# Optimization experiments

Measured on AMD Instinct MI355X. Metric: run time of the kernel, lower is better.

## Reference

```python
import jax, jax.numpy as jnp
import numpy as np

B, S, D = 4, 2048, 1024


def setup_inputs() -> dict:
    key = jax.random.key(0)
    ks = jax.random.split(key, 7)
    s = 1.0 / np.sqrt(D)
    return {
        "x": jax.random.normal(ks[0], (B, S, D), dtype=jnp.float32),
        "Wq": jax.random.normal(ks[1], (D, D), dtype=jnp.float32) * s,
        "bq": jax.random.normal(ks[2], (D,), dtype=jnp.float32) * s,
        "Wk": jax.random.normal(ks[3], (D, D), dtype=jnp.float32) * s,
        "bk": jax.random.normal(ks[4], (D,), dtype=jnp.float32) * s,
        "Wv": jax.random.normal(ks[5], (D, D), dtype=jnp.float32) * s,
        "bv": jax.random.normal(ks[6], (D,), dtype=jnp.float32) * s,
    }


def reference(x, Wq, bq, Wk, bk, Wv, bv):
    # Linear layers: y = x @ W^T + b (torch nn.Linear convention)
    Q = jnp.einsum("bsd,ed->bse", x, Wq) + bq  # [B,S,D]
    K = jnp.einsum("bsd,ed->bse", x, Wk) + bk
    V = jnp.einsum("bsd,ed->bse", x, Wv) + bv
    d = x.shape[-1]
    scores = jnp.einsum("bqd,bkd->bqk", Q, K) / jnp.sqrt(jnp.float32(d))  # [B,S,S]
    weights = jax.nn.softmax(scores, axis=-1)
    O = jnp.einsum("bqk,bkd->bqd", weights, V)  # [B,S,D]
    return O
```

## Files before the change

### kernel.cpp

```cpp
#include <hip/hip_runtime.h>

typedef __bf16 bf16x8 __attribute__((ext_vector_type(8)));
typedef __bf16 bf16x4 __attribute__((ext_vector_type(4)));
typedef float  f32x4  __attribute__((ext_vector_type(4)));

#define BM 128
#define BN 128
#define BK 32

__device__ __forceinline__ void gload_lds16(const __bf16* g, __bf16* l) {
  __builtin_amdgcn_global_load_lds(
      (const __attribute__((address_space(1))) void*)g,
      (__attribute__((address_space(3))) void*)l,
      16, 0, 0);
}

__global__ void cvt_f32_bf16(const float* __restrict__ s, __bf16* __restrict__ d, int n4) {
  int i = blockIdx.x * 256 + threadIdx.x;
  if (i < n4) {
    float4 v = ((const float4*)s)[i];
    bf16x4 o;
    o[0] = (__bf16)v.x; o[1] = (__bf16)v.y; o[2] = (__bf16)v.z; o[3] = (__bf16)v.w;
    ((bf16x4*)d)[i] = o;
  }
}

__global__ void cvt_weights(const float* __restrict__ Wq, const float* __restrict__ Wk,
                            const float* __restrict__ Wv,
                            __bf16* __restrict__ Wqk, __bf16* __restrict__ Wvb) {
  const int mat = blockIdx.x >> 10;
  const int i = (blockIdx.x & 1023) * 256 + threadIdx.x;
  const float* src = (mat == 0) ? Wq : (mat == 1) ? Wk : Wv;
  __bf16* dst = (mat == 0) ? Wqk : (mat == 1) ? (Wqk + 1048576) : Wvb;
  float4 v = ((const float4*)src)[i];
  bf16x4 o;
  o[0] = (__bf16)v.x; o[1] = (__bf16)v.y; o[2] = (__bf16)v.z; o[3] = (__bf16)v.w;
  ((bf16x4*)dst)[i] = o;
}

template<int MODE>
__global__ __launch_bounds__(256, 2)
void gemm_bt(const __bf16* __restrict__ A, const __bf16* __restrict__ B,
             float* __restrict__ C,
             int lda, int ldb, int ldc, int K,
             long sA, long sB, long sC,
             const float* __restrict__ bias0, const float* __restrict__ bias1,
             __bf16* __restrict__ out0, __bf16* __restrict__ out1)
{
  A += (long)blockIdx.z * sA;
  B += (long)blockIdx.z * sB;

  const int tid  = threadIdx.x;
  const int wave = tid >> 6;
  const int lane = tid & 63;
  const int quad = lane >> 4;
  const int l15  = lane & 15;
  const int bm0  = blockIdx.x * BM;
  const int bn0  = blockIdx.y * BN;
  const int wm   = (wave >> 1) * 64;
  const int wn   = (wave & 1) * 64;

  __shared__ __align__(16) __bf16 As[BM * BK];
  __shared__ __align__(16) __bf16 Bs[BN * BK];

  f32x4 acc[4][4];
#pragma unroll
  for (int i = 0; i < 4; ++i)
#pragma unroll
    for (int j = 0; j < 4; ++j)
      acc[i][j] = (f32x4){0.f, 0.f, 0.f, 0.f};

  const int l0 = tid * 8;
  const int l1 = (256 + tid) * 8;
  const int r0 = l0 >> 5, c0 = l0 & 31;
  const int r1 = l1 >> 5, c1 = l1 & 31;
  const __bf16* Ag0 = A + (size_t)(bm0 + r0) * lda + c0;
  const __bf16* Ag1 = A + (size_t)(bm0 + r1) * lda + c1;
  const __bf16* Bg0 = B + (size_t)(bn0 + r0) * ldb + c0;
  const __bf16* Bg1 = B + (size_t)(bn0 + r1) * ldb + c1;

  for (int k0 = 0; k0 < K; k0 += BK) {
    gload_lds16(Ag0 + k0, &As[l0]);
    gload_lds16(Ag1 + k0, &As[l1]);
    gload_lds16(Bg0 + k0, &Bs[l0]);
    gload_lds16(Bg1 + k0, &Bs[l1]);
    __syncthreads();

    bf16x8 af[4], bfv[4];
#pragma unroll
    for (int i = 0; i < 4; ++i)
      af[i] = *(const bf16x8*)&As[(wm + i * 16 + l15) * BK + quad * 8];
#pragma unroll
    for (int i = 0; i < 4; ++i)
      bfv[i] = *(const bf16x8*)&Bs[(wn + i * 16 + l15) * BK + quad * 8];

#pragma unroll
    for (int mi = 0; mi < 4; ++mi)
#pragma unroll
      for (int ni = 0; ni < 4; ++ni)
        acc[mi][ni] = __builtin_amdgcn_mfma_f32_16x16x32_bf16(
            af[mi], bfv[ni], acc[mi][ni], 0, 0, 0);
    __syncthreads();
  }

#pragma unroll
  for (int mi = 0; mi < 4; ++mi) {
#pragma unroll
    for (int ni = 0; ni < 4; ++ni) {
      const int gn = bn0 + wn + ni * 16 + l15;
#pragma unroll
      for (int r = 0; r < 4; ++r) {
        const int gm = bm0 + wm + mi * 16 + quad * 4 + r;
        float v = acc[mi][ni][r];
        if (MODE == 0) {
          const int mat = gn >> 10;
          const int d   = gn & 1023;
          const float* bias = (mat == 0) ? bias0 : bias1;
          __bf16* dst = (mat == 0) ? out0 : out1;
          dst[(size_t)gm * 1024 + d] = (__bf16)(v + bias[d]);
        } else if (MODE == 1) {
          const int b = gn >> 11, s = gn & 2047;
          out0[(size_t)b * (1024 * 2048) + (size_t)gm * 2048 + s] =
              (__bf16)(v + bias0[gm]);
        } else {
          C[(long)blockIdx.z * sC + (size_t)gm * ldc + gn] = v;
        }
      }
    }
  }
}

__global__ __launch_bounds__(256)
void softmax_rows(float* __restrict__ S) {
  float* row = S + (size_t)blockIdx.x * 2048;
  __bf16* wrow = (__bf16*)row;
  const int t = threadIdx.x;
  const int wave = t >> 6;
  const int lane = t & 63;
  __shared__ float redm[4];
  __shared__ float reds[4];

  float4 a = ((const float4*)row)[t];
  float4 b = ((const float4*)row)[t + 256];
  const float sc = 0.03125f;
  float x0 = a.x * sc, x1 = a.y * sc, x2 = a.z * sc, x3 = a.w * sc;
  float x4 = b.x * sc, x5 = b.y * sc, x6 = b.z * sc, x7 = b.w * sc;

  float mx = fmaxf(fmaxf(fmaxf(x0, x1), fmaxf(x2, x3)),
                   fmaxf(fmaxf(x4, x5), fmaxf(x6, x7)));
#pragma unroll
  for (int off = 32; off > 0; off >>= 1)
    mx = fmaxf(mx, __shfl_down(mx, off));
  if (lane == 0) redm[wave] = mx;
  __syncthreads();
  mx = fmaxf(fmaxf(redm[0], redm[1]), fmaxf(redm[2], redm[3]));

  float e0 = __expf(x0 - mx), e1 = __expf(x1 - mx);
  float e2 = __expf(x2 - mx), e3 = __expf(x3 - mx);
  float e4 = __expf(x4 - mx), e5 = __expf(x5 - mx);
  float e6 = __expf(x6 - mx), e7 = __expf(x7 - mx);
  float s = ((e0 + e1) + (e2 + e3)) + ((e4 + e5) + (e6 + e7));
#pragma unroll
  for (int off = 32; off > 0; off >>= 1)
    s += __shfl_down(s, off);
  if (lane == 0) reds[wave] = s;
  __syncthreads();
  const float rinv = 1.0f / (((reds[0] + reds[1]) + (reds[2] + reds[3])));

  bf16x4 w0, w1;
  w0[0] = (__bf16)(e0 * rinv); w0[1] = (__bf16)(e1 * rinv);
  w0[2] = (__bf16)(e2 * rinv); w0[3] = (__bf16)(e3 * rinv);
  w1[0] = (__bf16)(e4 * rinv); w1[1] = (__bf16)(e5 * rinv);
  w1[2] = (__bf16)(e6 * rinv); w1[3] = (__bf16)(e7 * rinv);
  ((bf16x4*)wrow)[t] = w0;
  ((bf16x4*)wrow)[t + 256] = w1;
}

extern "C" void kernel_launch(void* const* d_in, const int* in_sizes, int n_in,
                              void* d_out, int out_size, void* d_ws, size_t ws_size,
                              hipStream_t stream) {
  const float* x  = (const float*)d_in[0];
  const float* Wq = (const float*)d_in[1];
  const float* bq = (const float*)d_in[2];
  const float* Wk = (const float*)d_in[3];
  const float* bk = (const float*)d_in[4];
  const float* Wv = (const float*)d_in[5];
  const float* bv = (const float*)d_in[6];
  float* out = (float*)d_out;

  char* ws = (char*)d_ws;
  __bf16* Q    = (__bf16*)(ws);
  __bf16* Kb   = (__bf16*)(ws + (16ull << 20));
  __bf16* Vt   = (__bf16*)(ws + (32ull << 20));
  __bf16* xb   = (__bf16*)(ws + (48ull << 20));
  __bf16* Wqk  = (__bf16*)(ws + (64ull << 20));
  __bf16* Wvb  = (__bf16*)(ws + (68ull << 20));
  float*  Sc   = (float*)(ws + (48ull << 20));

  cvt_f32_bf16<<<8192, 256, 0, stream>>>(x, xb, 8388608 / 4);
  cvt_weights<<<3072, 256, 0, stream>>>(Wq, Wk, Wv, Wqk, Wvb);

  dim3 blk(256);
  gemm_bt<0><<<dim3(64, 16, 1), blk, 0, stream>>>(
      xb, Wqk, nullptr, 1024, 1024, 0, 1024,
      0L, 0L, 0L, bq, bk, Q, Kb);

  gemm_bt<1><<<dim3(8, 64, 1), blk, 0, stream>>>(
      Wvb, xb, nullptr, 1024, 1024, 0, 1024,
      0L, 0L, 0L, bv, nullptr, Vt, nullptr);

  gemm_bt<2><<<dim3(16, 16, 4), blk, 0, stream>>>(
      Q, Kb, Sc, 1024, 1024, 2048, 1024,
      2048L * 1024, 2048L * 1024, 2048L * 2048,
      nullptr, nullptr, nullptr, nullptr);

  softmax_rows<<<8192, 256, 0, stream>>>(Sc);

  gemm_bt<2><<<dim3(16, 8, 4), blk, 0, stream>>>(
      (const __bf16*)Sc, Vt, out, 4096, 2048, 1024, 2048,
      2048L * 4096, 1024L * 2048, 2048L * 1024,
      nullptr, nullptr, nullptr, nullptr);
}
```

Before: 283.0 us.

## Merge conversion and QKV projection launches, use narrower tiles for PV GEMM

```diff
diff --git a/kernel.cpp b/kernel.cpp
--- a/kernel.cpp
+++ b/kernel.cpp
@@ -15,23 +15,23 @@
       16, 0, 0);
 }
 
-__global__ void cvt_f32_bf16(const float* __restrict__ s, __bf16* __restrict__ d, int n4) {
-  int i = blockIdx.x * 256 + threadIdx.x;
-  if (i < n4) {
-    float4 v = ((const float4*)s)[i];
-    bf16x4 o;
-    o[0] = (__bf16)v.x; o[1] = (__bf16)v.y; o[2] = (__bf16)v.z; o[3] = (__bf16)v.w;
-    ((bf16x4*)d)[i] = o;
-  }
-}
-
-__global__ void cvt_weights(const float* __restrict__ Wq, const float* __restrict__ Wk,
-                            const float* __restrict__ Wv,
-                            __bf16* __restrict__ Wqk, __bf16* __restrict__ Wvb) {
-  const int mat = blockIdx.x >> 10;
-  const int i = (blockIdx.x & 1023) * 256 + threadIdx.x;
-  const float* src = (mat == 0) ? Wq : (mat == 1) ? Wk : Wv;
-  __bf16* dst = (mat == 0) ? Wqk : (mat == 1) ? (Wqk + 1048576) : Wvb;
+__global__ void cvt_all(const float* __restrict__ x, const float* __restrict__ Wq,
+                        const float* __restrict__ Wk, const float* __restrict__ Wv,
+                        __bf16* __restrict__ xb, __bf16* __restrict__ Wqk,
+                        __bf16* __restrict__ Wvb) {
+  int b = blockIdx.x;
+  const float* src;
+  __bf16* dst;
+  int i;
+  if (b < 8192) {
+    src = x; dst = xb; i = b * 256 + threadIdx.x;
+  } else {
+    b -= 8192;
+    const int mat = b >> 10;
+    i = (b & 1023) * 256 + threadIdx.x;
+    src = (mat == 0) ? Wq : (mat == 1) ? Wk : Wv;
+    dst = (mat == 0) ? Wqk : (mat == 1) ? (Wqk + 1048576) : Wvb;
+  }
   float4 v = ((const float4*)src)[i];
   bf16x4 o;
   o[0] = (__bf16)v.x; o[1] = (__bf16)v.y; o[2] = (__bf16)v.z; o[3] = (__bf16)v.w;
@@ -45,18 +45,30 @@
              int lda, int ldb, int ldc, int K,
              long sA, long sB, long sC,
              const float* __restrict__ bias0, const float* __restrict__ bias1,
-             __bf16* __restrict__ out0, __bf16* __restrict__ out1)
+             const float* __restrict__ bias2, const __bf16* __restrict__ Wvb,
+             __bf16* __restrict__ out0, __bf16* __restrict__ out1,
+             __bf16* __restrict__ out2)
 {
-  A += (long)blockIdx.z * sA;
-  B += (long)blockIdx.z * sB;
+  const __bf16* Ap = A + (long)blockIdx.z * sA;
+  const __bf16* Bp = B + (long)blockIdx.z * sB;
+
+  int bx, by;
+  if (MODE == 3) {
+    const int gid = blockIdx.x;
+    if (gid < 1024) { bx = gid & 63; by = gid >> 6; }
+    else { const int g = gid - 1024; bx = g & 7; by = g >> 3;
+           Ap = Wvb; Bp = A; }
+  } else {
+    bx = blockIdx.x; by = blockIdx.y;
+  }
 
   const int tid  = threadIdx.x;
   const int wave = tid >> 6;
   const int lane = tid & 63;
   const int quad = lane >> 4;
   const int l15  = lane & 15;
-  const int bm0  = blockIdx.x * BM;
-  const int bn0  = blockIdx.y * BN;
+  const int bm0  = bx * BM;
+  const int bn0  = by * BN;
   const int wm   = (wave >> 1) * 64;
   const int wn   = (wave & 1) * 64;
 
@@ -68,6 +80,96 @@
   for (int i = 0; i < 4; ++i)
 #pragma unroll
     for (int j = 0; j < 4; ++j)
+      acc[i][j] = (f32x4){0.f, 0.f, 0.f, 0.f};
+
+  const int l0 = tid * 8;
+  const int l1 = (256 + tid) * 8;
+  const int r0 = l0 >> 5, c0 = l0 & 31;
+  const int r1 = l1 >> 5, c1 = l1 & 31;
+  const __bf16* Ag0 = Ap + (size_t)(bm0 + r0) * lda + c0;
+  const __bf16* Ag1 = Ap + (size_t)(bm0 + r1) * lda + c1;
+  const __bf16* Bg0 = Bp + (size_t)(bn0 + r0) * ldb + c0;
+  const __bf16* Bg1 = Bp + (size_t)(bn0 + r1) * ldb + c1;
+
+  for (int k0 = 0; k0 < K; k0 += BK) {
+    gload_lds16(Ag0 + k0, &As[l0]);
+    gload_lds16(Ag1 + k0, &As[l1]);
+    gload_lds16(Bg0 + k0, &Bs[l0]);
+    gload_lds16(Bg1 + k0, &Bs[l1]);
+    __syncthreads();
+
+    bf16x8 af[4], bfv[4];
+#pragma unroll
+    for (int i = 0; i < 4; ++i)
+      af[i] = *(const bf16x8*)&As[(wm + i * 16 + l15) * BK + quad * 8];
+#pragma unroll
+    for (int i = 0; i < 4; ++i)
+      bfv[i] = *(const bf16x8*)&Bs[(wn + i * 16 + l15) * BK + quad * 8];
+
+#pragma unroll
+    for (int mi = 0; mi < 4; ++mi)
+#pragma unroll
+      for (int ni = 0; ni < 4; ++ni)
+        acc[mi][ni] = __builtin_amdgcn_mfma_f32_16x16x32_bf16(
+            af[mi], bfv[ni], acc[mi][ni], 0, 0, 0);
+    __syncthreads();
+  }
+
+#pragma unroll
+  for (int mi = 0; mi < 4; ++mi) {
+#pragma unroll
+    for (int ni = 0; ni < 4; ++ni) {
+      const int gn = bn0 + wn + ni * 16 + l15;
+#pragma unroll
+      for (int r = 0; r < 4; ++r) {
+        const int gm = bm0 + wm + mi * 16 + quad * 4 + r;
+        float v = acc[mi][ni][r];
+        if (MODE == 3) {
+          if (blockIdx.x < 1024) {
+            const int mat = gn >> 10;
+            const int d   = gn & 1023;
+            const float* bias = (mat == 0) ? bias0 : bias1;
+            __bf16* dst = (mat == 0) ? out0 : out1;
+            dst[(size_t)gm * 1024 + d] = (__bf16)(v + bias[d]);
+          } else {
+            const int b = gn >> 11, s = gn & 2047;
+            out2[(size_t)b * (1024 * 2048) + (size_t)gm * 2048 + s] =
+                (__bf16)(v + bias2[gm]);
+          }
+        } else {
+          C[(long)blockIdx.z * sC + (size_t)gm * ldc + gn] = v;
+        }
+      }
+    }
+  }
+}
+
+__global__ __launch_bounds__(256, 4)
+void gemm_pv(const __bf16* __restrict__ A, const __bf16* __restrict__ B,
+             float* __restrict__ C,
+             int lda, int ldb, int ldc, int K, long sA, long sB, long sC)
+{
+  A += (long)blockIdx.z * sA;
+  B += (long)blockIdx.z * sB;
+
+  const int tid  = threadIdx.x;
+  const int wave = tid >> 6;
+  const int lane = tid & 63;
+  const int quad = lane >> 4;
+  const int l15  = lane & 15;
+  const int bm0  = blockIdx.x * 128;
+  const int bn0  = blockIdx.y * 64;
+  const int wm   = (wave >> 1) * 64;
+  const int wn   = (wave & 1) * 32;
+
+  __shared__ __align__(16) __bf16 As[128 * BK];
+  __shared__ __align__(16) __bf16 Bs[64 * BK];
+
+  f32x4 acc[4][2];
+#pragma unroll
+  for (int i = 0; i < 4; ++i)
+#pragma unroll
+    for (int j = 0; j < 2; ++j)
       acc[i][j] = (f32x4){0.f, 0.f, 0.f, 0.f};
 
   const int l0 = tid * 8;
@@ -77,27 +179,25 @@
   const __bf16* Ag0 = A + (size_t)(bm0 + r0) * lda + c0;
   const __bf16* Ag1 = A + (size_t)(bm0 + r1) * lda + c1;
   const __bf16* Bg0 = B + (size_t)(bn0 + r0) * ldb + c0;
-  const __bf16* Bg1 = B + (size_t)(bn0 + r1) * ldb + c1;
 
   for (int k0 = 0; k0 < K; k0 += BK) {
     gload_lds16(Ag0 + k0, &As[l0]);
     gload_lds16(Ag1 + k0, &As[l1]);
     gload_lds16(Bg0 + k0, &Bs[l0]);
-    gload_lds16(Bg1 + k0, &Bs[l1]);
     __syncthreads();
 
-    bf16x8 af[4], bfv[4];
+    bf16x8 af[4], bfv[2];
 #pragma unroll
     for (int i = 0; i < 4; ++i)
       af[i] = *(const bf16x8*)&As[(wm + i * 16 + l15) * BK + quad * 8];
 #pragma unroll
-    for (int i = 0; i < 4; ++i)
+    for (int i = 0; i < 2; ++i)
       bfv[i] = *(const bf16x8*)&Bs[(wn + i * 16 + l15) * BK + quad * 8];
 
 #pragma unroll
     for (int mi = 0; mi < 4; ++mi)
 #pragma unroll
-      for (int ni = 0; ni < 4; ++ni)
+      for (int ni = 0; ni < 2; ++ni)
         acc[mi][ni] = __builtin_amdgcn_mfma_f32_16x16x32_bf16(
             af[mi], bfv[ni], acc[mi][ni], 0, 0, 0);
     __syncthreads();
@@ -106,25 +206,12 @@
 #pragma unroll
   for (int mi = 0; mi < 4; ++mi) {
 #pragma unroll
-    for (int ni = 0; ni < 4; ++ni) {
+    for (int ni = 0; ni < 2; ++ni) {
       const int gn = bn0 + wn + ni * 16 + l15;
 #pragma unroll
       for (int r = 0; r < 4; ++r) {
         const int gm = bm0 + wm + mi * 16 + quad * 4 + r;
-        float v = acc[mi][ni][r];
-        if (MODE == 0) {
-          const int mat = gn >> 10;
-          const int d   = gn & 1023;
-          const float* bias = (mat == 0) ? bias0 : bias1;
-          __bf16* dst = (mat == 0) ? out0 : out1;
-          dst[(size_t)gm * 1024 + d] = (__bf16)(v + bias[d]);
-        } else if (MODE == 1) {
-          const int b = gn >> 11, s = gn & 2047;
-          out0[(size_t)b * (1024 * 2048) + (size_t)gm * 2048 + s] =
-              (__bf16)(v + bias0[gm]);
-        } else {
-          C[(long)blockIdx.z * sC + (size_t)gm * ldc + gn] = v;
-        }
+        C[(long)blockIdx.z * sC + (size_t)gm * ldc + gn] = acc[mi][ni][r];
       }
     }
   }
@@ -197,27 +284,22 @@
   __bf16* Wvb  = (__bf16*)(ws + (68ull << 20));
   float*  Sc   = (float*)(ws + (48ull << 20));
 
-  cvt_f32_bf16<<<8192, 256, 0, stream>>>(x, xb, 8388608 / 4);
-  cvt_weights<<<3072, 256, 0, stream>>>(Wq, Wk, Wv, Wqk, Wvb);
-
   dim3 blk(256);
-  gemm_bt<0><<<dim3(64, 16, 1), blk, 0, stream>>>(
+
+  cvt_all<<<11264, blk, 0, stream>>>(x, Wq, Wk, Wv, xb, Wqk, Wvb);
+
+  gemm_bt<3><<<dim3(1536, 1, 1), blk, 0, stream>>>(
       xb, Wqk, nullptr, 1024, 1024, 0, 1024,
-      0L, 0L, 0L, bq, bk, Q, Kb);
-
-  gemm_bt<1><<<dim3(8, 64, 1), blk, 0, stream>>>(
-      Wvb, xb, nullptr, 1024, 1024, 0, 1024,
-      0L, 0L, 0L, bv, nullptr, Vt, nullptr);
+      0L, 0L, 0L, bq, bk, bv, Wvb, Q, Kb, Vt);
 
   gemm_bt<2><<<dim3(16, 16, 4), blk, 0, stream>>>(
       Q, Kb, Sc, 1024, 1024, 2048, 1024,
       2048L * 1024, 2048L * 1024, 2048L * 2048,
-      nullptr, nullptr, nullptr, nullptr);
-
-  softmax_rows<<<8192, 256, 0, stream>>>(Sc);
-
-  gemm_bt<2><<<dim3(16, 8, 4), blk, 0, stream>>>(
+      nullptr, nullptr, nullptr, nullptr, nullptr, nullptr, nullptr);
+
+  softmax_rows<<<8192, blk, 0, stream>>>(Sc);
+
+  gemm_pv<<<dim3(16, 16, 4), blk, 0, stream>>>(
       (const __bf16*)Sc, Vt, out, 4096, 2048, 1024, 2048,
-      2048L * 4096, 1024L * 2048, 2048L * 1024,
-      nullptr, nullptr, nullptr, nullptr);
-}
+      2048L * 4096, 1024L * 2048, 2048L * 1024);
+}
```

Result: slower. 299.0 us (+5.7%).

## Fuse all attention stages into one persistent kernel with grid barriers

Applied to the files above, without the earlier changes.

```diff
diff --git a/kernel.cpp b/kernel.cpp
--- a/kernel.cpp
+++ b/kernel.cpp
@@ -7,6 +7,7 @@
 #define BM 128
 #define BN 128
 #define BK 32
+#define NBLK 512
 
 __device__ __forceinline__ void gload_lds16(const __bf16* g, __bf16* l) {
   __builtin_amdgcn_global_load_lds(
@@ -15,53 +16,36 @@
       16, 0, 0);
 }
 
-__global__ void cvt_f32_bf16(const float* __restrict__ s, __bf16* __restrict__ d, int n4) {
-  int i = blockIdx.x * 256 + threadIdx.x;
-  if (i < n4) {
-    float4 v = ((const float4*)s)[i];
-    bf16x4 o;
-    o[0] = (__bf16)v.x; o[1] = (__bf16)v.y; o[2] = (__bf16)v.z; o[3] = (__bf16)v.w;
-    ((bf16x4*)d)[i] = o;
-  }
-}
-
-__global__ void cvt_weights(const float* __restrict__ Wq, const float* __restrict__ Wk,
-                            const float* __restrict__ Wv,
-                            __bf16* __restrict__ Wqk, __bf16* __restrict__ Wvb) {
-  const int mat = blockIdx.x >> 10;
-  const int i = (blockIdx.x & 1023) * 256 + threadIdx.x;
-  const float* src = (mat == 0) ? Wq : (mat == 1) ? Wk : Wv;
-  __bf16* dst = (mat == 0) ? Wqk : (mat == 1) ? (Wqk + 1048576) : Wvb;
-  float4 v = ((const float4*)src)[i];
-  bf16x4 o;
-  o[0] = (__bf16)v.x; o[1] = (__bf16)v.y; o[2] = (__bf16)v.z; o[3] = (__bf16)v.w;
-  ((bf16x4*)dst)[i] = o;
+__device__ __forceinline__ void grid_bar(unsigned* ctr, unsigned epoch) {
+  __syncthreads();
+  if (threadIdx.x == 0) {
+    __threadfence();
+    __hip_atomic_fetch_add(ctr, 1u, __ATOMIC_RELEASE, __HIP_MEMORY_SCOPE_AGENT);
+    while (__hip_atomic_load(ctr, __ATOMIC_RELAXED, __HIP_MEMORY_SCOPE_AGENT) <
+           epoch * NBLK) {
+      __builtin_amdgcn_s_sleep(8);
+    }
+    __threadfence();
+  }
+  __syncthreads();
 }
 
 template<int MODE>
-__global__ __launch_bounds__(256, 2)
-void gemm_bt(const __bf16* __restrict__ A, const __bf16* __restrict__ B,
-             float* __restrict__ C,
-             int lda, int ldb, int ldc, int K,
-             long sA, long sB, long sC,
-             const float* __restrict__ bias0, const float* __restrict__ bias1,
-             __bf16* __restrict__ out0, __bf16* __restrict__ out1)
+__device__ __forceinline__ void gemm_tile(
+    const __bf16* __restrict__ Ap, const __bf16* __restrict__ Bp,
+    float* __restrict__ C, int lda, int ldb, int ldc, int K,
+    int bm0, int bn0,
+    const float* __restrict__ bias0, const float* __restrict__ bias1,
+    __bf16* __restrict__ out0, __bf16* __restrict__ out1,
+    __bf16* As, __bf16* Bs)
 {
-  A += (long)blockIdx.z * sA;
-  B += (long)blockIdx.z * sB;
-
   const int tid  = threadIdx.x;
   const int wave = tid >> 6;
   const int lane = tid & 63;
   const int quad = lane >> 4;
   const int l15  = lane & 15;
-  const int bm0  = blockIdx.x * BM;
-  const int bn0  = blockIdx.y * BN;
   const int wm   = (wave >> 1) * 64;
   const int wn   = (wave & 1) * 64;
-
-  __shared__ __align__(16) __bf16 As[BM * BK];
-  __shared__ __align__(16) __bf16 Bs[BN * BK];
 
   f32x4 acc[4][4];
 #pragma unroll
@@ -74,10 +58,10 @@
   const int l1 = (256 + tid) * 8;
   const int r0 = l0 >> 5, c0 = l0 & 31;
   const int r1 = l1 >> 5, c1 = l1 & 31;
-  const __bf16* Ag0 = A + (size_t)(bm0 + r0) * lda + c0;
-  const __bf16* Ag1 = A + (size_t)(bm0 + r1) * lda + c1;
-  const __bf16* Bg0 = B + (size_t)(bn0 + r0) * ldb + c0;
-  const __bf16* Bg1 = B + (size_t)(bn0 + r1) * ldb + c1;
+  const __bf16* Ag0 = Ap + (size_t)(bm0 + r0) * lda + c0;
+  const __bf16* Ag1 = Ap + (size_t)(bm0 + r1) * lda + c1;
+  const __bf16* Bg0 = Bp + (size_t)(bn0 + r0) * ldb + c0;
+  const __bf16* Bg1 = Bp + (size_t)(bn0 + r1) * ldb + c1;
 
   for (int k0 = 0; k0 < K; k0 += BK) {
     gload_lds16(Ag0 + k0, &As[l0]);
@@ -123,22 +107,20 @@
           out0[(size_t)b * (1024 * 2048) + (size_t)gm * 2048 + s] =
               (__bf16)(v + bias0[gm]);
         } else {
-          C[(long)blockIdx.z * sC + (size_t)gm * ldc + gn] = v;
+          C[(size_t)gm * ldc + gn] = v;
         }
       }
     }
   }
 }
 
-__global__ __launch_bounds__(256)
-void softmax_rows(float* __restrict__ S) {
-  float* row = S + (size_t)blockIdx.x * 2048;
+__device__ __forceinline__ void softmax_row(float* __restrict__ row, float* red) {
   __bf16* wrow = (__bf16*)row;
   const int t = threadIdx.x;
   const int wave = t >> 6;
   const int lane = t & 63;
-  __shared__ float redm[4];
-  __shared__ float reds[4];
+  float* redm = red;
+  float* reds = red + 4;
 
   float4 a = ((const float4*)row)[t];
   float4 b = ((const float4*)row)[t + 256];
@@ -174,6 +156,80 @@
   w1[2] = (__bf16)(e6 * rinv); w1[3] = (__bf16)(e7 * rinv);
   ((bf16x4*)wrow)[t] = w0;
   ((bf16x4*)wrow)[t + 256] = w1;
+  __syncthreads();
+}
+
+__global__ __launch_bounds__(256, 2)
+void attn_mega(const float* __restrict__ x, const float* __restrict__ Wq,
+               const float* __restrict__ Wk, const float* __restrict__ Wv,
+               const float* __restrict__ bq, const float* __restrict__ bk,
+               const float* __restrict__ bv, float* __restrict__ out,
+               char* __restrict__ ws)
+{
+  __bf16* Q    = (__bf16*)(ws);
+  __bf16* Kb   = (__bf16*)(ws + (16ull << 20));
+  __bf16* Vt   = (__bf16*)(ws + (32ull << 20));
+  __bf16* xb   = (__bf16*)(ws + (48ull << 20));
+  __bf16* Wqk  = (__bf16*)(ws + (64ull << 20));
+  __bf16* Wvb  = (__bf16*)(ws + (68ull << 20));
+  float*  Sc   = (float*)(ws + (48ull << 20));
+  unsigned* ctrA = (unsigned*)(ws + (112ull << 20) - 128);
+  unsigned* ctrB = (unsigned*)((char*)out + (32ull << 20) - 128);
+
+  __shared__ __align__(16) __bf16 As[BM * BK];
+  __shared__ __align__(16) __bf16 Bs[BN * BK];
+
+  for (int u = blockIdx.x; u < 11264; u += NBLK) {
+    const float* src; __bf16* dst; int i;
+    if (u < 8192) {
+      src = x; dst = xb; i = u * 256 + threadIdx.x;
+    } else {
+      const int b = u - 8192;
+      const int mat = b >> 10;
+      i = (b & 1023) * 256 + threadIdx.x;
+      src = (mat == 0) ? Wq : (mat == 1) ? Wk : Wv;
+      dst = (mat == 0) ? Wqk : (mat == 1) ? (Wqk + 1048576) : Wvb;
+    }
+    float4 v = ((const float4*)src)[i];
+    bf16x4 o;
+    o[0] = (__bf16)v.x; o[1] = (__bf16)v.y; o[2] = (__bf16)v.z; o[3] = (__bf16)v.w;
+    ((bf16x4*)dst)[i] = o;
+  }
+  grid_bar(ctrA, 1);
+
+  for (int t = blockIdx.x; t < 1536; t += NBLK) {
+    if (t < 1024) {
+      gemm_tile<0>(xb, Wqk, nullptr, 1024, 1024, 0, 1024,
+                   (t & 63) * BM, (t >> 6) * BN, bq, bk, Q, Kb, As, Bs);
+    } else {
+      const int g = t - 1024;
+      gemm_tile<1>(Wvb, xb, nullptr, 1024, 1024, 0, 1024,
+                   (g & 7) * BM, (g >> 3) * BN, bv, nullptr, Vt, nullptr, As, Bs);
+    }
+  }
+  grid_bar(ctrA, 2);
+
+  for (int t = blockIdx.x; t < 1024; t += NBLK) {
+    const int z = t >> 8, rem = t & 255;
+    gemm_tile<2>(Q + (size_t)z * 2048 * 1024, Kb + (size_t)z * 2048 * 1024,
+                 Sc + (size_t)z * 2048 * 2048, 1024, 1024, 2048, 1024,
+                 (rem & 15) * BM, (rem >> 4) * BN,
+                 nullptr, nullptr, nullptr, nullptr, As, Bs);
+  }
+  grid_bar(ctrB, 1);
+
+  for (int r = blockIdx.x; r < 8192; r += NBLK)
+    softmax_row(Sc + (size_t)r * 2048, (float*)As);
+  grid_bar(ctrB, 2);
+
+  for (int t = blockIdx.x; t < 512; t += NBLK) {
+    const int z = t >> 7, rem = t & 127;
+    gemm_tile<2>((const __bf16*)Sc + (size_t)z * 2048 * 4096,
+                 Vt + (size_t)z * 1024 * 2048,
+                 out + (size_t)z * 2048 * 1024, 4096, 2048, 1024, 2048,
+                 (rem & 15) * BM, (rem >> 4) * BN,
+                 nullptr, nullptr, nullptr, nullptr, As, Bs);
+  }
 }
 
 extern "C" void kernel_launch(void* const* d_in, const int* in_sizes, int n_in,
@@ -187,37 +243,11 @@
   const float* Wv = (const float*)d_in[5];
   const float* bv = (const float*)d_in[6];
   float* out = (float*)d_out;
-
   char* ws = (char*)d_ws;
-  __bf16* Q    = (__bf16*)(ws);
-  __bf16* Kb   = (__bf16*)(ws + (16ull << 20));
-  __bf16* Vt   = (__bf16*)(ws + (32ull << 20));
-  __bf16* xb   = (__bf16*)(ws + (48ull << 20));
-  __bf16* Wqk  = (__bf16*)(ws + (64ull << 20));
-  __bf16* Wvb  = (__bf16*)(ws + (68ull << 20));
-  float*  Sc   = (float*)(ws + (48ull << 20));
-
-  cvt_f32_bf16<<<8192, 256, 0, stream>>>(x, xb, 8388608 / 4);
-  cvt_weights<<<3072, 256, 0, stream>>>(Wq, Wk, Wv, Wqk, Wvb);
-
-  dim3 blk(256);
-  gemm_bt<0><<<dim3(64, 16, 1), blk, 0, stream>>>(
-      xb, Wqk, nullptr, 1024, 1024, 0, 1024,
-      0L, 0L, 0L, bq, bk, Q, Kb);
-
-  gemm_bt<1><<<dim3(8, 64, 1), blk, 0, stream>>>(
-      Wvb, xb, nullptr, 1024, 1024, 0, 1024,
-      0L, 0L, 0L, bv, nullptr, Vt, nullptr);
-
-  gemm_bt<2><<<dim3(16, 16, 4), blk, 0, stream>>>(
-      Q, Kb, Sc, 1024, 1024, 2048, 1024,
-      2048L * 1024, 2048L * 1024, 2048L * 2048,
-      nullptr, nullptr, nullptr, nullptr);
-
-  softmax_rows<<<8192, 256, 0, stream>>>(Sc);
-
-  gemm_bt<2><<<dim3(16, 8, 4), blk, 0, stream>>>(
-      (const __bf16*)Sc, Vt, out, 4096, 2048, 1024, 2048,
-      2048L * 4096, 1024L * 2048, 2048L * 1024,
-      nullptr, nullptr, nullptr, nullptr);
-}
+
+  hipMemsetAsync(ws + (112ull << 20) - 128, 0, 128, stream);
+  hipMemsetAsync((char*)out + (32ull << 20) - 128, 0, 128, stream);
+
+  attn_mega<<<dim3(NBLK), dim3(256), 0, stream>>>(
+      x, Wq, Wk, Wv, bq, bk, bv, out, ws);
+}
```

After: 568.3 us. 2.01x slower.

## Fuse softmax into QK and PV GEMM epilogues, merge conversion kernels

Applied to the files above, without the earlier changes.

```diff
diff --git a/kernel.cpp b/kernel.cpp
--- a/kernel.cpp
+++ b/kernel.cpp
@@ -1,8 +1,8 @@
 #include <hip/hip_runtime.h>
 
-typedef __bf16 bf16x8 __attribute__((ext_vector_type(8)));
-typedef __bf16 bf16x4 __attribute__((ext_vector_type(4)));
-typedef float  f32x4  __attribute__((ext_vector_type(4)));
+typedef __bf16    bf16x8 __attribute__((ext_vector_type(8)));
+typedef __bf16    bf16x4 __attribute__((ext_vector_type(4)));
+typedef float     f32x4  __attribute__((ext_vector_type(4)));
 
 #define BM 128
 #define BN 128
@@ -15,23 +15,26 @@
       16, 0, 0);
 }
 
-__global__ void cvt_f32_bf16(const float* __restrict__ s, __bf16* __restrict__ d, int n4) {
-  int i = blockIdx.x * 256 + threadIdx.x;
-  if (i < n4) {
-    float4 v = ((const float4*)s)[i];
-    bf16x4 o;
-    o[0] = (__bf16)v.x; o[1] = (__bf16)v.y; o[2] = (__bf16)v.z; o[3] = (__bf16)v.w;
-    ((bf16x4*)d)[i] = o;
-  }
-}
-
-__global__ void cvt_weights(const float* __restrict__ Wq, const float* __restrict__ Wk,
-                            const float* __restrict__ Wv,
-                            __bf16* __restrict__ Wqk, __bf16* __restrict__ Wvb) {
-  const int mat = blockIdx.x >> 10;
-  const int i = (blockIdx.x & 1023) * 256 + threadIdx.x;
-  const float* src = (mat == 0) ? Wq : (mat == 1) ? Wk : Wv;
-  __bf16* dst = (mat == 0) ? Wqk : (mat == 1) ? (Wqk + 1048576) : Wvb;
+__global__ void cvt_all(const float* __restrict__ x, const float* __restrict__ Wq,
+                        const float* __restrict__ Wk, const float* __restrict__ Wv,
+                        __bf16* __restrict__ xb, __bf16* __restrict__ Wqk,
+                        __bf16* __restrict__ Wvb, float* __restrict__ lsum) {
+  int b = blockIdx.x;
+  if (b == 0) {
+    for (int j = threadIdx.x; j < 8192; j += 256) lsum[j] = 0.f;
+  }
+  const float* src;
+  __bf16* dst;
+  int i;
+  if (b < 8192) {
+    src = x; dst = xb; i = b * 256 + threadIdx.x;
+  } else {
+    b -= 8192;
+    const int mat = b >> 10;
+    i = (b & 1023) * 256 + threadIdx.x;
+    src = (mat == 0) ? Wq : (mat == 1) ? Wk : Wv;
+    dst = (mat == 0) ? Wqk : (mat == 1) ? (Wqk + 1048576) : Wvb;
+  }
   float4 v = ((const float4*)src)[i];
   bf16x4 o;
   o[0] = (__bf16)v.x; o[1] = (__bf16)v.y; o[2] = (__bf16)v.z; o[3] = (__bf16)v.w;
@@ -45,6 +48,7 @@
              int lda, int ldb, int ldc, int K,
              long sA, long sB, long sC,
              const float* __restrict__ bias0, const float* __restrict__ bias1,
+             float* __restrict__ lsum,
              __bf16* __restrict__ out0, __bf16* __restrict__ out1)
 {
   A += (long)blockIdx.z * sA;
@@ -103,77 +107,67 @@
     __syncthreads();
   }
 
-#pragma unroll
-  for (int mi = 0; mi < 4; ++mi) {
-#pragma unroll
-    for (int ni = 0; ni < 4; ++ni) {
-      const int gn = bn0 + wn + ni * 16 + l15;
+  if (MODE == 2) {
+#pragma unroll
+    for (int mi = 0; mi < 4; ++mi) {
 #pragma unroll
       for (int r = 0; r < 4; ++r) {
         const int gm = bm0 + wm + mi * 16 + quad * 4 + r;
-        float v = acc[mi][ni][r];
-        if (MODE == 0) {
-          const int mat = gn >> 10;
-          const int d   = gn & 1023;
-          const float* bias = (mat == 0) ? bias0 : bias1;
-          __bf16* dst = (mat == 0) ? out0 : out1;
-          dst[(size_t)gm * 1024 + d] = (__bf16)(v + bias[d]);
-        } else if (MODE == 1) {
-          const int b = gn >> 11, s = gn & 2047;
-          out0[(size_t)b * (1024 * 2048) + (size_t)gm * 2048 + s] =
-              (__bf16)(v + bias0[gm]);
-        } else {
-          C[(long)blockIdx.z * sC + (size_t)gm * ldc + gn] = v;
+        float part = 0.f;
+#pragma unroll
+        for (int ni = 0; ni < 4; ++ni) {
+          const int gn = bn0 + wn + ni * 16 + l15;
+          const __bf16 eb = (__bf16)__expf(acc[mi][ni][r] * 0.03125f);
+          out0[(long)blockIdx.z * sC + (size_t)gm * ldc + gn] = eb;
+          part += (float)eb;
+        }
+        part += __shfl_xor(part, 1);
+        part += __shfl_xor(part, 2);
+        part += __shfl_xor(part, 4);
+        part += __shfl_xor(part, 8);
+        if (l15 == 0)
+          atomicAdd(&lsum[blockIdx.z * 2048 + gm], part);
+      }
+    }
+  } else if (MODE == 3) {
+#pragma unroll
+    for (int mi = 0; mi < 4; ++mi) {
+#pragma unroll
+      for (int r = 0; r < 4; ++r) {
+        const int gm = bm0 + wm + mi * 16 + quad * 4 + r;
+        const float rv = 1.0f / lsum[blockIdx.z * 2048 + gm];
+#pragma unroll
+        for (int ni = 0; ni < 4; ++ni) {
+          const int gn = bn0 + wn + ni * 16 + l15;
+          C[(long)blockIdx.z * sC + (size_t)gm * ldc + gn] = acc[mi][ni][r] * rv;
         }
       }
     }
-  }
-}
-
-__global__ __launch_bounds__(256)
-void softmax_rows(float* __restrict__ S) {
-  float* row = S + (size_t)blockIdx.x * 2048;
-  __bf16* wrow = (__bf16*)row;
-  const int t = threadIdx.x;
-  const int wave = t >> 6;
-  const int lane = t & 63;
-  __shared__ float redm[4];
-  __shared__ float reds[4];
-
-  float4 a = ((const float4*)row)[t];
-  float4 b = ((const float4*)row)[t + 256];
-  const float sc = 0.03125f;
-  float x0 = a.x * sc, x1 = a.y * sc, x2 = a.z * sc, x3 = a.w * sc;
-  float x4 = b.x * sc, x5 = b.y * sc, x6 = b.z * sc, x7 = b.w * sc;
-
-  float mx = fmaxf(fmaxf(fmaxf(x0, x1), fmaxf(x2, x3)),
-                   fmaxf(fmaxf(x4, x5), fmaxf(x6, x7)));
-#pragma unroll
-  for (int off = 32; off > 0; off >>= 1)
-    mx = fmaxf(mx, __shfl_down(mx, off));
-  if (lane == 0) redm[wave] = mx;
-  __syncthreads();
-  mx = fmaxf(fmaxf(redm[0], redm[1]), fmaxf(redm[2], redm[3]));
-
-  float e0 = __expf(x0 - mx), e1 = __expf(x1 - mx);
-  float e2 = __expf(x2 - mx), e3 = __expf(x3 - mx);
-  float e4 = __expf(x4 - mx), e5 = __expf(x5 - mx);
-  float e6 = __expf(x6 - mx), e7 = __expf(x7 - mx);
-  float s = ((e0 + e1) + (e2 + e3)) + ((e4 + e5) + (e6 + e7));
-#pragma unroll
-  for (int off = 32; off > 0; off >>= 1)
-    s += __shfl_down(s, off);
-  if (lane == 0) reds[wave] = s;
-  __syncthreads();
-  const float rinv = 1.0f / (((reds[0] + reds[1]) + (reds[2] + reds[3])));
-
-  bf16x4 w0, w1;
-  w0[0] = (__bf16)(e0 * rinv); w0[1] = (__bf16)(e1 * rinv);
-  w0[2] = (__bf16)(e2 * rinv); w0[3] = (__bf16)(e3 * rinv);
-  w1[0] = (__bf16)(e4 * rinv); w1[1] = (__bf16)(e5 * rinv);
-  w1[2] = (__bf16)(e6 * rinv); w1[3] = (__bf16)(e7 * rinv);
-  ((bf16x4*)wrow)[t] = w0;
-  ((bf16x4*)wrow)[t + 256] = w1;
+  } else {
+#pragma unroll
+    for (int mi = 0; mi < 4; ++mi) {
+#pragma unroll
+      for (int ni = 0; ni < 4; ++ni) {
+        const int gn = bn0 + wn + ni * 16 + l15;
+#pragma unroll
+        for (int r = 0; r < 4; ++r) {
+          const int gm = bm0 + wm + mi * 16 + quad * 4 + r;
+          float v = acc[mi][ni][r];
+          if (MODE == 0) {
+            const int mat = gn >> 10;
+            const int d   = gn & 1023;
+            const float* bias = (mat == 0) ? bias0 : bias1;
+            __bf16* dst = (mat == 0) ? out0 : out1;
+            dst[(size_t)gm * 1024 + d] = (__bf16)(v + bias[d]);
+          } else {
+            const int b = gn >> 11, s = gn & 2047;
+            out0[(size_t)b * (1024 * 2048) + (size_t)gm * 2048 + s] =
+                (__bf16)(v + bias0[gm]);
+          }
+        }
+      }
+    }
+  }
 }
 
 extern "C" void kernel_launch(void* const* d_in, const int* in_sizes, int n_in,
@@ -195,29 +189,28 @@
   __bf16* xb   = (__bf16*)(ws + (48ull << 20));
   __bf16* Wqk  = (__bf16*)(ws + (64ull << 20));
   __bf16* Wvb  = (__bf16*)(ws + (68ull << 20));
-  float*  Sc   = (float*)(ws + (48ull << 20));
-
-  cvt_f32_bf16<<<8192, 256, 0, stream>>>(x, xb, 8388608 / 4);
-  cvt_weights<<<3072, 256, 0, stream>>>(Wq, Wk, Wv, Wqk, Wvb);
+  __bf16* Sc   = (__bf16*)(ws + (48ull << 20));
+  float*  lsum = (float*)(ws + (110ull << 20));
 
   dim3 blk(256);
+
+  cvt_all<<<11264, blk, 0, stream>>>(x, Wq, Wk, Wv, xb, Wqk, Wvb, lsum);
+
   gemm_bt<0><<<dim3(64, 16, 1), blk, 0, stream>>>(
       xb, Wqk, nullptr, 1024, 1024, 0, 1024,
-      0L, 0L, 0L, bq, bk, Q, Kb);
+      0L, 0L, 0L, bq, bk, nullptr, Q, Kb);
 
   gemm_bt<1><<<dim3(8, 64, 1), blk, 0, stream>>>(
       Wvb, xb, nullptr, 1024, 1024, 0, 1024,
-      0L, 0L, 0L, bv, nullptr, Vt, nullptr);
+      0L, 0L, 0L, bv, nullptr, nullptr, Vt, nullptr);
 
   gemm_bt<2><<<dim3(16, 16, 4), blk, 0, stream>>>(
-      Q, Kb, Sc, 1024, 1024, 2048, 1024,
+      Q, Kb, nullptr, 1024, 1024, 2048, 1024,
       2048L * 1024, 2048L * 1024, 2048L * 2048,
-      nullptr, nullptr, nullptr, nullptr);
-
-  softmax_rows<<<8192, 256, 0, stream>>>(Sc);
-
-  gemm_bt<2><<<dim3(16, 8, 4), blk, 0, stream>>>(
-      (const __bf16*)Sc, Vt, out, 4096, 2048, 1024, 2048,
-      2048L * 4096, 1024L * 2048, 2048L * 1024,
-      nullptr, nullptr, nullptr, nullptr);
-}
+      nullptr, nullptr, lsum, Sc, nullptr);
+
+  gemm_bt<3><<<dim3(16, 8, 4), blk, 0, stream>>>(
+      Sc, Vt, out, 2048, 2048, 1024, 2048,
+      2048L * 2048, 1024L * 2048, 2048L * 1024,
+      nullptr, nullptr, lsum, nullptr, nullptr);
+}
```

Measured after the change: 268.9 us. 1.05x faster.
